# Optimization experiments

Measured on AMD Instinct MI355X. Metric: run time of the kernel, lower is better.

The kernel has to match this reference:

```python
import jax, jax.numpy as jnp
import numpy as np

N_NODES = 50000


def gcn_conv(x, W, b, src, dst, n):
    # dense transform first (as PyG GCNConv does), then sparse aggregate
    h = x @ W  # [N, out]
    # add self loops
    loop = jnp.arange(n, dtype=src.dtype)
    s = jnp.concatenate([src, loop])
    d = jnp.concatenate([dst, loop])
    # symmetric normalization: deg over targets with unit edge weights
    deg = jax.ops.segment_sum(jnp.ones_like(d, dtype=h.dtype), d, num_segments=n)
    dinv = jnp.where(deg > 0, jax.lax.rsqrt(deg), 0.0)
    norm = dinv[s] * dinv[d]  # [E+N]
    msg = h[s] * norm[:, None]  # gather + scale
    out = jax.ops.segment_sum(msg, d, num_segments=n)  # scatter-add
    return out + b


def setup_inputs() -> dict:
    key = jax.random.key(0)
    k1, k2, k3, k4, k5 = jax.random.split(key, 5)
    in_dim, hid, out_dim = 256, 128, 16
    x = jax.random.normal(k1, (N_NODES, in_dim), dtype=jnp.float32)
    edge_index = jax.random.randint(k2, (2, 800000), 0, N_NODES, dtype=jnp.int64)
    # Glorot-style init for GCNConv weights, zero bias (PyG default)
    W1 = jax.random.normal(k3, (in_dim, hid), dtype=jnp.float32) / np.sqrt(in_dim)
    b1 = jnp.zeros((hid,), dtype=jnp.float32)
    W2 = jax.random.normal(k4, (hid, out_dim), dtype=jnp.float32) / np.sqrt(hid)
    b2 = jnp.zeros((out_dim,), dtype=jnp.float32)
    return {"x": x, "edge_index": edge_index, "W1": W1, "b1": b1, "W2": W2, "b2": b2}


def reference(x, edge_index, W1, b1, W2, b2):
    # eval-mode forward: dropout is identity
    src, dst = edge_index[0], edge_index[1]
    n = x.shape[0]
    h = gcn_conv(x, W1, b1, src, dst, n)
    h = jax.nn.relu(h)
    h = gcn_conv(h, W2, b2, src, dst, n)
    return jax.nn.log_softmax(h, axis=1)
```

## Files before the change

### kernel.cpp

```cpp
#include <hip/hip_runtime.h>
#include <hip/hip_bf16.h>

#define N_NODES 50000
#define E_EDGES 800000
#define IN_DIM  256
#define HID     128
#define OUT_DIM 16

#define NBUCK 391
#define NBLK  128
#define P2CAP 4096

using frag_ab = __attribute__((ext_vector_type(8))) short;
using frag_cd = __attribute__((ext_vector_type(4))) float;

static __device__ inline short f2bf(float f) {
    union { float f; unsigned u; } v; v.f = f;
    unsigned r = (v.u + 0x7fffu + ((v.u >> 16) & 1u)) >> 16;
    return (short)r;
}
static __device__ inline float bflo(unsigned u) {
    union { unsigned u; float f; } v; v.u = u << 16; return v.f;
}
static __device__ inline float bfhi(unsigned u) {
    union { unsigned u; float f; } v; v.u = u & 0xffff0000u; return v.f;
}
static __device__ inline unsigned packbf(float a, float b) {
    return (unsigned)(unsigned short)f2bf(a) | ((unsigned)(unsigned short)f2bf(b) << 16);
}


__global__ __launch_bounds__(256) void csr_a(const int4* __restrict__ dst4,
                                             int* __restrict__ cnt_bb) {
    __shared__ int h[NBUCK];
    int t = threadIdx.x;
    for (int i = t; i < NBUCK; i += 256) h[i] = 0;
    __syncthreads();
    for (int i = blockIdx.x * 256 + t; i < E_EDGES / 4; i += NBLK * 256) {
        int4 d = dst4[i];
        atomicAdd(&h[d.x >> 7], 1);
        atomicAdd(&h[d.y >> 7], 1);
        atomicAdd(&h[d.z >> 7], 1);
        atomicAdd(&h[d.w >> 7], 1);
    }
    __syncthreads();
    for (int i = t; i < NBUCK; i += 256) cnt_bb[i * NBLK + blockIdx.x] = h[i];
}

__global__ __launch_bounds__(NBLK) void csr_b1(int* __restrict__ cnt_bb,
                                               int* __restrict__ btot) {
    __shared__ int sm[NBLK];
    int b = blockIdx.x, t = threadIdx.x;
    int v = cnt_bb[b * NBLK + t];
    sm[t] = v;
    __syncthreads();
    for (int o = 1; o < NBLK; o <<= 1) {
        int u = (t >= o) ? sm[t - o] : 0;
        __syncthreads();
        sm[t] += u;
        __syncthreads();
    }
    cnt_bb[b * NBLK + t] = sm[t] - v;
    if (t == NBLK - 1) btot[b] = sm[t];
}

__global__ __launch_bounds__(512) void csr_b2_w1t(const int* __restrict__ btot,
                                                  int* __restrict__ bbase,
                                                  const float* __restrict__ W,
                                                  uint4* __restrict__ wtf,
                                                  const float* __restrict__ W2,
                                                  short* __restrict__ w2t) {
    int t = threadIdx.x;
    if (blockIdx.x < 8) {
        int j = blockIdx.x * 512 + t;
        int f = j >> 6, lane = j & 63;
        int kt = f >> 3, tt = f & 7;
        int m = lane & 15, q = lane >> 4;
        int c = tt * 16 + m;
        int k0 = kt * 32 + q * 8;
        unsigned p[4];
#pragma unroll
        for (int i = 0; i < 4; ++i)
            p[i] = packbf(W[(k0 + 2 * i) * HID + c], W[(k0 + 2 * i + 1) * HID + c]);
        uint4 v; v.x = p[0]; v.y = p[1]; v.z = p[2]; v.w = p[3];
        wtf[j] = v;
        return;
    }
    if (blockIdx.x == 9) {
        int n0 = t >> 5, k0 = (t & 31) * 4;
#pragma unroll
        for (int i = 0; i < 4; ++i)
            w2t[n0 * HID + k0 + i] = f2bf(W2[(k0 + i) * OUT_DIM + n0]);
        return;
    }
    __shared__ int sm[512];
    int v = (t < NBUCK) ? btot[t] : 0;
    sm[t] = v;
    __syncthreads();
    for (int o = 1; o < 512; o <<= 1) {
        int u = (t >= o) ? sm[t - o] : 0;
        __syncthreads();
        sm[t] += u;
        __syncthreads();
    }
    if (t < NBUCK) bbase[t] = sm[t] - v;
    if (t == 511) bbase[NBUCK] = sm[511];
}

__global__ __launch_bounds__(256) void csr_c(const int4* __restrict__ src4,
                                             const int4* __restrict__ dst4,
                                             const int* __restrict__ cnt_bb,
                                             const int* __restrict__ bbase,
                                             unsigned* __restrict__ tmp) {
    __shared__ int run[NBUCK];
    int t = threadIdx.x;
    for (int i = t; i < NBUCK; i += 256)
        run[i] = bbase[i] + cnt_bb[i * NBLK + blockIdx.x];
    __syncthreads();
    for (int i = blockIdx.x * 256 + t; i < E_EDGES / 4; i += NBLK * 256) {
        int4 d = dst4[i];
        int4 s = src4[i];
        int p0 = atomicAdd(&run[d.x >> 7], 1);
        tmp[p0] = (unsigned)s.x | ((unsigned)(d.x & 127) << 17);
        int p1 = atomicAdd(&run[d.y >> 7], 1);
        tmp[p1] = (unsigned)s.y | ((unsigned)(d.y & 127) << 17);
        int p2 = atomicAdd(&run[d.z >> 7], 1);
        tmp[p2] = (unsigned)s.z | ((unsigned)(d.z & 127) << 17);
        int p3 = atomicAdd(&run[d.w >> 7], 1);
        tmp[p3] = (unsigned)s.w | ((unsigned)(d.w & 127) << 17);
    }
}

__global__ __launch_bounds__(256) void csr_p2(const unsigned* __restrict__ tmp,
                                              const int* __restrict__ bbase,
                                              int* __restrict__ rowptr,
                                              float* __restrict__ dinv,
                                              int* __restrict__ ssrc) {
    __shared__ unsigned ed[P2CAP];
    __shared__ int cnt[128];
    __shared__ int off[128];
    int b = blockIdx.x, t = threadIdx.x;
    int base = bbase[b];
    int m = bbase[b + 1] - base;
    if (m > P2CAP) m = P2CAP;
    if (t < 128) cnt[t] = 0;
    __syncthreads();
    for (int i = t; i < m; i += 256) {
        unsigned v = tmp[base + i];
        ed[i] = v;
        atomicAdd(&cnt[v >> 17], 1);
    }
    __syncthreads();
    if (t < 128) off[t] = cnt[t];
    __syncthreads();
    for (int o = 1; o < 128; o <<= 1) {
        int u = (t >= o && t < 128) ? off[t - o] : 0;
        __syncthreads();
        if (t < 128) off[t] += u;
        __syncthreads();
    }
    if (t < 128) {
        int node = b * 128 + t;
        int ex = off[t] - cnt[t];
        if (node < N_NODES) {
            rowptr[node] = base + ex;
            dinv[node] = rsqrtf((float)(cnt[t] + 1));
        }
        off[t] = ex;
    }
    if (b == NBUCK - 1 && t == 0) rowptr[N_NODES] = E_EDGES;
    __syncthreads();
    for (int i = t; i < m; i += 256) {
        unsigned v = ed[i];
        int p = atomicAdd(&off[v >> 17], 1);
        ssrc[base + p] = (int)(v & 0x1FFFF);
    }
}

__global__ __launch_bounds__(512) void gemm1_mfma(const float* __restrict__ x,
                                                  const uint4* __restrict__ wtf,
                                                  const float* __restrict__ dinv,
                                                  short* __restrict__ h) {
    __shared__ uint4 lwt[64 * 64];
    int tid = threadIdx.x;
#pragma unroll
    for (int i = 0; i < 8; ++i)
        lwt[i * 512 + tid] = wtf[i * 512 + tid];

    int wave = tid >> 6;
    int lane = tid & 63;
    int m = lane & 15;
    int q = lane >> 4;
    int row0 = blockIdx.x * 128 + wave * 16;
    int arow_idx = row0 + m;
    const float4* arow4 = (const float4*)(x + (size_t)(arow_idx < N_NODES ? arow_idx : 0) * IN_DIM);

    frag_ab a[8];
#pragma unroll
    for (int kt = 0; kt < 8; ++kt) {
        float4 f0 = arow4[kt * 8 + q * 2];
        float4 f1 = arow4[kt * 8 + q * 2 + 1];
        a[kt][0] = f2bf(f0.x); a[kt][1] = f2bf(f0.y); a[kt][2] = f2bf(f0.z); a[kt][3] = f2bf(f0.w);
        a[kt][4] = f2bf(f1.x); a[kt][5] = f2bf(f1.y); a[kt][6] = f2bf(f1.z); a[kt][7] = f2bf(f1.w);
    }

    frag_cd acc[8];
#pragma unroll
    for (int t = 0; t < 8; ++t) acc[t] = frag_cd{0.f, 0.f, 0.f, 0.f};

    __syncthreads();

#pragma unroll
    for (int kt = 0; kt < 8; ++kt) {
#pragma unroll
        for (int t = 0; t < 8; ++t) {
            frag_ab b = *(const frag_ab*)&lwt[(kt * 8 + t) * 64 + lane];
            acc[t] = __builtin_amdgcn_mfma_f32_16x16x32_bf16(a[kt], b, acc[t], 0, 0, 0);
        }
    }

    float dv[4];
#pragma unroll
    for (int r = 0; r < 4; ++r) {
        int orow = row0 + q * 4 + r;
        dv[r] = (orow < N_NODES) ? dinv[orow] : 0.f;
    }
#pragma unroll
    for (int t = 0; t < 8; ++t) {
#pragma unroll
        for (int r = 0; r < 4; ++r) {
            int orow = row0 + q * 4 + r;
            if (orow < N_NODES)
                h[(size_t)orow * HID + t * 16 + m] = f2bf(acc[t][r] * dv[r]);
        }
    }
}

__global__ __launch_bounds__(256) void agg1_pull(const short* __restrict__ h1s,
                                                 const float* __restrict__ dinv,
                                                 const float* __restrict__ b1,
                                                 const int* __restrict__ rowptr,
                                                 const int* __restrict__ ssrc,
                                                 uint4* __restrict__ out1) {
    int wave = threadIdx.x >> 6;
    int lane = threadIdx.x & 63;
    int slot  = blockIdx.x & 7;
    int nb    = blockIdx.x >> 3;
    int slice = slot >> 1;
    int half  = slot & 1;
    int node = __builtin_amdgcn_readfirstlane(nb * 8 + half * 4 + wave);
    if (node >= N_NODES) return;
    int eo = lane >> 2;
    int g  = lane & 3;

    const short* base = h1s + slice * 32 + g * 8;
    int lo = rowptr[node], hi = rowptr[node + 1];
    float dd = dinv[node];
    float a0 = 0.f, a1 = 0.f, a2 = 0.f, a3 = 0.f;
    float a4 = 0.f, a5 = 0.f, a6 = 0.f, a7 = 0.f;

    if (eo == 0) {
        uint4 u = *(const uint4*)(base + (size_t)node * HID);
        a0 = bflo(u.x); a1 = bfhi(u.x); a2 = bflo(u.y); a3 = bfhi(u.y);
        a4 = bflo(u.z); a5 = bfhi(u.z); a6 = bflo(u.w); a7 = bfhi(u.w);
    }

    int e = lo;
    for (; e + 32 <= hi; e += 32) {
        int s0 = ssrc[e + eo];
        int s1 = ssrc[e + 16 + eo];
        uint4 u0 = *(const uint4*)(base + (size_t)s0 * HID);
        uint4 u1 = *(const uint4*)(base + (size_t)s1 * HID);
        a0 += bflo(u0.x); a1 += bfhi(u0.x); a2 += bflo(u0.y); a3 += bfhi(u0.y);
        a4 += bflo(u0.z); a5 += bfhi(u0.z); a6 += bflo(u0.w); a7 += bfhi(u0.w);
        a0 += bflo(u1.x); a1 += bfhi(u1.x); a2 += bflo(u1.y); a3 += bfhi(u1.y);
        a4 += bflo(u1.z); a5 += bfhi(u1.z); a6 += bflo(u1.w); a7 += bfhi(u1.w);
    }
    for (; e + 16 <= hi; e += 16) {
        int s = ssrc[e + eo];
        uint4 u = *(const uint4*)(base + (size_t)s * HID);
        a0 += bflo(u.x); a1 += bfhi(u.x); a2 += bflo(u.y); a3 += bfhi(u.y);
        a4 += bflo(u.z); a5 += bfhi(u.z); a6 += bflo(u.w); a7 += bfhi(u.w);
    }
    if (eo < hi - e) {
        int s = ssrc[e + eo];
        uint4 u = *(const uint4*)(base + (size_t)s * HID);
        a0 += bflo(u.x); a1 += bfhi(u.x); a2 += bflo(u.y); a3 += bfhi(u.y);
        a4 += bflo(u.z); a5 += bfhi(u.z); a6 += bflo(u.w); a7 += bfhi(u.w);
    }

#pragma unroll
    for (int msk = 4; msk <= 32; msk <<= 1) {
        a0 += __shfl_xor(a0, msk); a1 += __shfl_xor(a1, msk);
        a2 += __shfl_xor(a2, msk); a3 += __shfl_xor(a3, msk);
        a4 += __shfl_xor(a4, msk); a5 += __shfl_xor(a5, msk);
        a6 += __shfl_xor(a6, msk); a7 += __shfl_xor(a7, msk);
    }

    if (eo == 0) {
        const float* bs = b1 + slice * 32 + g * 8;
        float4 bA = *(const float4*)bs;
        float4 bB = *(const float4*)(bs + 4);
        float o0 = fmaxf(fmaf(dd, a0, bA.x), 0.f);
        float o1 = fmaxf(fmaf(dd, a1, bA.y), 0.f);
        float o2 = fmaxf(fmaf(dd, a2, bA.z), 0.f);
        float o3 = fmaxf(fmaf(dd, a3, bA.w), 0.f);
        float o4 = fmaxf(fmaf(dd, a4, bB.x), 0.f);
        float o5 = fmaxf(fmaf(dd, a5, bB.y), 0.f);
        float o6 = fmaxf(fmaf(dd, a6, bB.z), 0.f);
        float o7 = fmaxf(fmaf(dd, a7, bB.w), 0.f);
        uint4 st;
        st.x = packbf(o0, o1); st.y = packbf(o2, o3);
        st.z = packbf(o4, o5); st.w = packbf(o6, o7);
        out1[(size_t)node * 16 + slice * 4 + g] = st;
    }
}

__global__ __launch_bounds__(256) void gemm2_mfma(const short* __restrict__ out1,
                                                  const short* __restrict__ w2t,
                                                  const float* __restrict__ dinv,
                                                  short* __restrict__ h2s) {
    int wave = threadIdx.x >> 6;
    int lane = threadIdx.x & 63;
    int m = lane & 15;
    int q = lane >> 4;
    int row0 = blockIdx.x * 64 + wave * 16;
    int arow = row0 + m;
    if (arow >= N_NODES) arow = N_NODES - 1;
    const short* ap = out1 + (size_t)arow * HID + q * 8;
    const short* bp = w2t + m * HID + q * 8;

    frag_cd acc = frag_cd{0.f, 0.f, 0.f, 0.f};
#pragma unroll
    for (int kt = 0; kt < 4; ++kt) {
        frag_ab a = *(const frag_ab*)(ap + kt * 32);
        frag_ab b = *(const frag_ab*)(bp + kt * 32);
        acc = __builtin_amdgcn_mfma_f32_16x16x32_bf16(a, b, acc, 0, 0, 0);
    }
#pragma unroll
    for (int r = 0; r < 4; ++r) {
        int row = row0 + q * 4 + r;
        if (row < N_NODES)
            h2s[(size_t)row * OUT_DIM + m] = f2bf(acc[r] * dinv[row]);
    }
}

__global__ __launch_bounds__(256) void agg2_pull(const unsigned* __restrict__ h2s,
                                                 const float* __restrict__ dinv,
                                                 const float* __restrict__ b2,
                                                 const int* __restrict__ rowptr,
                                                 const int* __restrict__ ssrc,
                                                 float* __restrict__ out) {
    int wave = threadIdx.x >> 6;
    int lane = threadIdx.x & 63;
    int node = __builtin_amdgcn_readfirstlane(blockIdx.x * 4 + wave);
    if (node >= N_NODES) return;
    int eo = lane >> 3;
    int g  = lane & 7;

    int lo = rowptr[node], hi = rowptr[node + 1];
    float a0 = 0.f, a1 = 0.f;
    if (eo == 0) {
        unsigned u = h2s[(size_t)node * 8 + g];
        a0 = bflo(u); a1 = bfhi(u);
    }
    int e = lo;
    for (; e + 16 <= hi; e += 16) {
        int s0 = ssrc[e + eo];
        int s1 = ssrc[e + 8 + eo];
        unsigned u0 = h2s[(size_t)s0 * 8 + g];
        unsigned u1 = h2s[(size_t)s1 * 8 + g];
        a0 += bflo(u0); a1 += bfhi(u0);
        a0 += bflo(u1); a1 += bfhi(u1);
    }
    for (; e + 8 <= hi; e += 8) {
        int s = ssrc[e + eo];
        unsigned u = h2s[(size_t)s * 8 + g];
        a0 += bflo(u); a1 += bfhi(u);
    }
    if (eo < hi - e) {
        int s = ssrc[e + eo];
        unsigned u = h2s[(size_t)s * 8 + g];
        a0 += bflo(u); a1 += bfhi(u);
    }

    a0 += __shfl_xor(a0, 8);  a1 += __shfl_xor(a1, 8);
    a0 += __shfl_xor(a0, 16); a1 += __shfl_xor(a1, 16);
    a0 += __shfl_xor(a0, 32); a1 += __shfl_xor(a1, 32);

    float dd = dinv[node];
    float2 bb = *(const float2*)(b2 + 2 * g);
    float v0 = fmaf(dd, a0, bb.x);
    float v1 = fmaf(dd, a1, bb.y);

    float m = fmaxf(v0, v1);
#pragma unroll
    for (int msk = 1; msk < 8; msk <<= 1) m = fmaxf(m, __shfl_xor(m, msk));
    float s2 = __expf(v0 - m) + __expf(v1 - m);
#pragma unroll
    for (int msk = 1; msk < 8; msk <<= 1) s2 += __shfl_xor(s2, msk);
    float lse = m + __logf(s2);
    if (eo == 0) {
        float2 o; o.x = v0 - lse; o.y = v1 - lse;
        *(float2*)(out + (size_t)node * OUT_DIM + 2 * g) = o;
    }
}

extern "C" void kernel_launch(void* const* d_in, const int* in_sizes, int n_in,
                              void* d_out, int out_size, void* d_ws, size_t ws_size,
                              hipStream_t stream) {
    const float* x  = (const float*)d_in[0];
    const int*   ei = (const int*)d_in[1];
    const float* W1 = (const float*)d_in[2];
    const float* b1 = (const float*)d_in[3];
    const float* W2 = (const float*)d_in[4];
    const float* b2 = (const float*)d_in[5];
    float* out = (float*)d_out;

    const int n = N_NODES;
    const int e = E_EDGES;
    const int* srcp = ei;
    const int* dstp = ei + e;

    char* w = (char*)d_ws;
    int*      cnt_bb = (int*)w;        w += (size_t)NBUCK * NBLK * 4;
    int*      btot   = (int*)w;        w += (size_t)NBUCK * 4;
    int*      bbase  = (int*)w;        w += (size_t)(NBUCK + 1) * 4;
    int*      rowptr = (int*)w;        w += (size_t)(n + 1) * 4;
    float*    dinv   = (float*)w;      w += (size_t)n * 4;
    unsigned* tmp    = (unsigned*)w;   w += (size_t)e * 4;
    int*      ssrc   = (int*)w;        w += (size_t)e * 4;
    uint4*    wtf    = (uint4*)w;      w += (size_t)64 * 64 * 16;
    short*    w2t    = (short*)w;      w += (size_t)OUT_DIM * HID * 2;
    short*    h1s    = (short*)w;      w += (size_t)n * HID * 2;
    short*    out1   = (short*)w;      w += (size_t)n * HID * 2;
    short*    h2s    = (short*)w;      w += (size_t)n * OUT_DIM * 2;

    auto blk = [](long long total, int b) { return (int)((total + b - 1) / b); };

    csr_a<<<NBLK, 256, 0, stream>>>((const int4*)dstp, cnt_bb);
    csr_b1<<<NBUCK, NBLK, 0, stream>>>(cnt_bb, btot);
    csr_b2_w1t<<<10, 512, 0, stream>>>(btot, bbase, W1, wtf, W2, w2t);
    csr_c<<<NBLK, 256, 0, stream>>>((const int4*)srcp, (const int4*)dstp, cnt_bb, bbase, tmp);
    csr_p2<<<NBUCK, 256, 0, stream>>>(tmp, bbase, rowptr, dinv, ssrc);

    gemm1_mfma<<<blk(n, 128), 512, 0, stream>>>(x, wtf, dinv, h1s);
    agg1_pull<<<6250 * 8, 256, 0, stream>>>(h1s, dinv, b1, rowptr, ssrc, (uint4*)out1);

    gemm2_mfma<<<blk(n, 64), 256, 0, stream>>>(out1, w2t, dinv, h2s);
    agg2_pull<<<blk(n, 4), 256, 0, stream>>>((const unsigned*)h2s, dinv, b2, rowptr, ssrc, out);
}
```

Before: 226.8 us.

## Rework aggregation kernels: full-row gathers for node pairs, wider agg2 loads

agg1_pull now has each wave handle two nodes, with 16 lanes covering a full 128-wide bf16 row. Previously eight blocks each covered a 32-column slice of a node. This cuts redundant rowptr/ssrc reads and the launch count, and gives each edge a full 256-byte contiguous gather, but only 4 edges per node are in flight per iteration. agg2_pull switches to 8-byte loads with 16 edges per iteration and does the 16-wide softmax across 4 lanes.

```diff
diff --git a/kernel.cpp b/kernel.cpp
--- a/kernel.cpp
+++ b/kernel.cpp
@@ -244,75 +244,97 @@
                                                  uint4* __restrict__ out1) {
     int wave = threadIdx.x >> 6;
     int lane = threadIdx.x & 63;
-    int slot  = blockIdx.x & 7;
-    int nb    = blockIdx.x >> 3;
-    int slice = slot >> 1;
-    int half  = slot & 1;
-    int node = __builtin_amdgcn_readfirstlane(nb * 8 + half * 4 + wave);
-    if (node >= N_NODES) return;
-    int eo = lane >> 2;
-    int g  = lane & 3;
-
-    const short* base = h1s + slice * 32 + g * 8;
-    int lo = rowptr[node], hi = rowptr[node + 1];
-    float dd = dinv[node];
+    int pair = __builtin_amdgcn_readfirstlane(blockIdx.x * 4 + wave);
+    int n0 = pair * 2;
+    if (n0 >= N_NODES) return;
+    int n1 = n0 + 1;
+    int eo = lane >> 4;
+    int g  = lane & 15;
+
+    int lo0 = rowptr[n0];
+    int mid = rowptr[n0 + 1];
+    int hi1 = rowptr[n1 + 1];
+    float dd0 = dinv[n0], dd1 = dinv[n1];
+
     float a0 = 0.f, a1 = 0.f, a2 = 0.f, a3 = 0.f;
     float a4 = 0.f, a5 = 0.f, a6 = 0.f, a7 = 0.f;
+    float c0 = 0.f, c1 = 0.f, c2 = 0.f, c3 = 0.f;
+    float c4 = 0.f, c5 = 0.f, c6 = 0.f, c7 = 0.f;
 
     if (eo == 0) {
-        uint4 u = *(const uint4*)(base + (size_t)node * HID);
+        uint4 u = *(const uint4*)(h1s + (size_t)n0 * HID + g * 8);
         a0 = bflo(u.x); a1 = bfhi(u.x); a2 = bflo(u.y); a3 = bfhi(u.y);
         a4 = bflo(u.z); a5 = bfhi(u.z); a6 = bflo(u.w); a7 = bfhi(u.w);
-    }
-
-    int e = lo;
-    for (; e + 32 <= hi; e += 32) {
-        int s0 = ssrc[e + eo];
-        int s1 = ssrc[e + 16 + eo];
-        uint4 u0 = *(const uint4*)(base + (size_t)s0 * HID);
-        uint4 u1 = *(const uint4*)(base + (size_t)s1 * HID);
+    } else if (eo == 1) {
+        uint4 u = *(const uint4*)(h1s + (size_t)n1 * HID + g * 8);
+        c0 = bflo(u.x); c1 = bfhi(u.x); c2 = bflo(u.y); c3 = bfhi(u.y);
+        c4 = bflo(u.z); c5 = bfhi(u.z); c6 = bflo(u.w); c7 = bfhi(u.w);
+    }
+
+    int e0 = lo0, e1 = mid;
+    for (; e0 + 4 <= mid && e1 + 4 <= hi1; e0 += 4, e1 += 4) {
+        int s0 = ssrc[e0 + eo];
+        int s1 = ssrc[e1 + eo];
+        uint4 u0 = *(const uint4*)(h1s + (size_t)s0 * HID + g * 8);
+        uint4 u1 = *(const uint4*)(h1s + (size_t)s1 * HID + g * 8);
         a0 += bflo(u0.x); a1 += bfhi(u0.x); a2 += bflo(u0.y); a3 += bfhi(u0.y);
         a4 += bflo(u0.z); a5 += bfhi(u0.z); a6 += bflo(u0.w); a7 += bfhi(u0.w);
-        a0 += bflo(u1.x); a1 += bfhi(u1.x); a2 += bflo(u1.y); a3 += bfhi(u1.y);
-        a4 += bflo(u1.z); a5 += bfhi(u1.z); a6 += bflo(u1.w); a7 += bfhi(u1.w);
-    }
-    for (; e + 16 <= hi; e += 16) {
-        int s = ssrc[e + eo];
-        uint4 u = *(const uint4*)(base + (size_t)s * HID);
+        c0 += bflo(u1.x); c1 += bfhi(u1.x); c2 += bflo(u1.y); c3 += bfhi(u1.y);
+        c4 += bflo(u1.z); c5 += bfhi(u1.z); c6 += bflo(u1.w); c7 += bfhi(u1.w);
+    }
+    for (; e0 + 4 <= mid; e0 += 4) {
+        int s = ssrc[e0 + eo];
+        uint4 u = *(const uint4*)(h1s + (size_t)s * HID + g * 8);
         a0 += bflo(u.x); a1 += bfhi(u.x); a2 += bflo(u.y); a3 += bfhi(u.y);
         a4 += bflo(u.z); a5 += bfhi(u.z); a6 += bflo(u.w); a7 += bfhi(u.w);
     }
-    if (eo < hi - e) {
-        int s = ssrc[e + eo];
-        uint4 u = *(const uint4*)(base + (size_t)s * HID);
+    for (; e1 + 4 <= hi1; e1 += 4) {
+        int s = ssrc[e1 + eo];
+        uint4 u = *(const uint4*)(h1s + (size_t)s * HID + g * 8);
+        c0 += bflo(u.x); c1 += bfhi(u.x); c2 += bflo(u.y); c3 += bfhi(u.y);
+        c4 += bflo(u.z); c5 += bfhi(u.z); c6 += bflo(u.w); c7 += bfhi(u.w);
+    }
+    if (eo < mid - e0) {
+        int s = ssrc[e0 + eo];
+        uint4 u = *(const uint4*)(h1s + (size_t)s * HID + g * 8);
         a0 += bflo(u.x); a1 += bfhi(u.x); a2 += bflo(u.y); a3 += bfhi(u.y);
         a4 += bflo(u.z); a5 += bfhi(u.z); a6 += bflo(u.w); a7 += bfhi(u.w);
     }
-
-#pragma unroll
-    for (int msk = 4; msk <= 32; msk <<= 1) {
+    if (eo < hi1 - e1) {
+        int s = ssrc[e1 + eo];
+        uint4 u = *(const uint4*)(h1s + (size_t)s * HID + g * 8);
+        c0 += bflo(u.x); c1 += bfhi(u.x); c2 += bflo(u.y); c3 += bfhi(u.y);
+        c4 += bflo(u.z); c5 += bfhi(u.z); c6 += bflo(u.w); c7 += bfhi(u.w);
+    }
+
+#pragma unroll
+    for (int msk = 16; msk <= 32; msk <<= 1) {
         a0 += __shfl_xor(a0, msk); a1 += __shfl_xor(a1, msk);
         a2 += __shfl_xor(a2, msk); a3 += __shfl_xor(a3, msk);
         a4 += __shfl_xor(a4, msk); a5 += __shfl_xor(a5, msk);
         a6 += __shfl_xor(a6, msk); a7 += __shfl_xor(a7, msk);
-    }
-
+        c0 += __shfl_xor(c0, msk); c1 += __shfl_xor(c1, msk);
+        c2 += __shfl_xor(c2, msk); c3 += __shfl_xor(c3, msk);
+        c4 += __shfl_xor(c4, msk); c5 += __shfl_xor(c5, msk);
+        c6 += __shfl_xor(c6, msk); c7 += __shfl_xor(c7, msk);
+    }
+
+    float4 bA = *(const float4*)(b1 + g * 8);
+    float4 bB = *(const float4*)(b1 + g * 8 + 4);
     if (eo == 0) {
-        const float* bs = b1 + slice * 32 + g * 8;
-        float4 bA = *(const float4*)bs;
-        float4 bB = *(const float4*)(bs + 4);
-        float o0 = fmaxf(fmaf(dd, a0, bA.x), 0.f);
-        float o1 = fmaxf(fmaf(dd, a1, bA.y), 0.f);
-        float o2 = fmaxf(fmaf(dd, a2, bA.z), 0.f);
-        float o3 = fmaxf(fmaf(dd, a3, bA.w), 0.f);
-        float o4 = fmaxf(fmaf(dd, a4, bB.x), 0.f);
-        float o5 = fmaxf(fmaf(dd, a5, bB.y), 0.f);
-        float o6 = fmaxf(fmaf(dd, a6, bB.z), 0.f);
-        float o7 = fmaxf(fmaf(dd, a7, bB.w), 0.f);
         uint4 st;
-        st.x = packbf(o0, o1); st.y = packbf(o2, o3);
-        st.z = packbf(o4, o5); st.w = packbf(o6, o7);
-        out1[(size_t)node * 16 + slice * 4 + g] = st;
+        st.x = packbf(fmaxf(fmaf(dd0, a0, bA.x), 0.f), fmaxf(fmaf(dd0, a1, bA.y), 0.f));
+        st.y = packbf(fmaxf(fmaf(dd0, a2, bA.z), 0.f), fmaxf(fmaf(dd0, a3, bA.w), 0.f));
+        st.z = packbf(fmaxf(fmaf(dd0, a4, bB.x), 0.f), fmaxf(fmaf(dd0, a5, bB.y), 0.f));
+        st.w = packbf(fmaxf(fmaf(dd0, a6, bB.z), 0.f), fmaxf(fmaf(dd0, a7, bB.w), 0.f));
+        out1[(size_t)n0 * 16 + g] = st;
+    } else if (eo == 1) {
+        uint4 st;
+        st.x = packbf(fmaxf(fmaf(dd1, c0, bA.x), 0.f), fmaxf(fmaf(dd1, c1, bA.y), 0.f));
+        st.y = packbf(fmaxf(fmaf(dd1, c2, bA.z), 0.f), fmaxf(fmaf(dd1, c3, bA.w), 0.f));
+        st.z = packbf(fmaxf(fmaf(dd1, c4, bB.x), 0.f), fmaxf(fmaf(dd1, c5, bB.y), 0.f));
+        st.w = packbf(fmaxf(fmaf(dd1, c6, bB.z), 0.f), fmaxf(fmaf(dd1, c7, bB.w), 0.f));
+        out1[(size_t)n1 * 16 + g] = st;
     }
 }
 
@@ -345,7 +367,7 @@
     }
 }
 
-__global__ __launch_bounds__(256) void agg2_pull(const unsigned* __restrict__ h2s,
+__global__ __launch_bounds__(256) void agg2_pull(const uint2* __restrict__ h2s2,
                                                  const float* __restrict__ dinv,
                                                  const float* __restrict__ b2,
                                                  const int* __restrict__ rowptr,
@@ -355,54 +377,50 @@
     int lane = threadIdx.x & 63;
     int node = __builtin_amdgcn_readfirstlane(blockIdx.x * 4 + wave);
     if (node >= N_NODES) return;
-    int eo = lane >> 3;
-    int g  = lane & 7;
+    int eo = lane >> 2;
+    int g  = lane & 3;
 
     int lo = rowptr[node], hi = rowptr[node + 1];
-    float a0 = 0.f, a1 = 0.f;
+    float a0 = 0.f, a1 = 0.f, a2 = 0.f, a3 = 0.f;
     if (eo == 0) {
-        unsigned u = h2s[(size_t)node * 8 + g];
-        a0 = bflo(u); a1 = bfhi(u);
+        uint2 u = h2s2[(size_t)node * 4 + g];
+        a0 = bflo(u.x); a1 = bfhi(u.x); a2 = bflo(u.y); a3 = bfhi(u.y);
     }
     int e = lo;
     for (; e + 16 <= hi; e += 16) {
-        int s0 = ssrc[e + eo];
-        int s1 = ssrc[e + 8 + eo];
-        unsigned u0 = h2s[(size_t)s0 * 8 + g];
-        unsigned u1 = h2s[(size_t)s1 * 8 + g];
-        a0 += bflo(u0); a1 += bfhi(u0);
-        a0 += bflo(u1); a1 += bfhi(u1);
-    }
-    for (; e + 8 <= hi; e += 8) {
         int s = ssrc[e + eo];
-        unsigned u = h2s[(size_t)s * 8 + g];
-        a0 += bflo(u); a1 += bfhi(u);
+        uint2 u = h2s2[(size_t)s * 4 + g];
+        a0 += bflo(u.x); a1 += bfhi(u.x); a2 += bflo(u.y); a3 += bfhi(u.y);
     }
     if (eo < hi - e) {
         int s = ssrc[e + eo];
-        unsigned u = h2s[(size_t)s * 8 + g];
-        a0 += bflo(u); a1 += bfhi(u);
-    }
-
-    a0 += __shfl_xor(a0, 8);  a1 += __shfl_xor(a1, 8);
-    a0 += __shfl_xor(a0, 16); a1 += __shfl_xor(a1, 16);
-    a0 += __shfl_xor(a0, 32); a1 += __shfl_xor(a1, 32);
+        uint2 u = h2s2[(size_t)s * 4 + g];
+        a0 += bflo(u.x); a1 += bfhi(u.x); a2 += bflo(u.y); a3 += bfhi(u.y);
+    }
+
+#pragma unroll
+    for (int msk = 4; msk <= 32; msk <<= 1) {
+        a0 += __shfl_xor(a0, msk); a1 += __shfl_xor(a1, msk);
+        a2 += __shfl_xor(a2, msk); a3 += __shfl_xor(a3, msk);
+    }
 
     float dd = dinv[node];
-    float2 bb = *(const float2*)(b2 + 2 * g);
+    float4 bb = *(const float4*)(b2 + 4 * g);
     float v0 = fmaf(dd, a0, bb.x);
     float v1 = fmaf(dd, a1, bb.y);
-
-    float m = fmaxf(v0, v1);
-#pragma unroll
-    for (int msk = 1; msk < 8; msk <<= 1) m = fmaxf(m, __shfl_xor(m, msk));
-    float s2 = __expf(v0 - m) + __expf(v1 - m);
-#pragma unroll
-    for (int msk = 1; msk < 8; msk <<= 1) s2 += __shfl_xor(s2, msk);
-    float lse = m + __logf(s2);
+    float v2 = fmaf(dd, a2, bb.z);
+    float v3 = fmaf(dd, a3, bb.w);
+
+    float m = fmaxf(fmaxf(v0, v1), fmaxf(v2, v3));
+    m = fmaxf(m, __shfl_xor(m, 1));
+    m = fmaxf(m, __shfl_xor(m, 2));
+    float s4 = __expf(v0 - m) + __expf(v1 - m) + __expf(v2 - m) + __expf(v3 - m);
+    s4 += __shfl_xor(s4, 1);
+    s4 += __shfl_xor(s4, 2);
+    float lse = m + __logf(s4);
     if (eo == 0) {
-        float2 o; o.x = v0 - lse; o.y = v1 - lse;
-        *(float2*)(out + (size_t)node * OUT_DIM + 2 * g) = o;
+        float4 o; o.x = v0 - lse; o.y = v1 - lse; o.z = v2 - lse; o.w = v3 - lse;
+        *(float4*)(out + (size_t)node * OUT_DIM + 4 * g) = o;
     }
 }
 
@@ -445,8 +463,8 @@
     csr_p2<<<NBUCK, 256, 0, stream>>>(tmp, bbase, rowptr, dinv, ssrc);
 
     gemm1_mfma<<<blk(n, 128), 512, 0, stream>>>(x, wtf, dinv, h1s);
-    agg1_pull<<<6250 * 8, 256, 0, stream>>>(h1s, dinv, b1, rowptr, ssrc, (uint4*)out1);
+    agg1_pull<<<blk(n / 2, 4), 256, 0, stream>>>(h1s, dinv, b1, rowptr, ssrc, (uint4*)out1);
 
     gemm2_mfma<<<blk(n, 64), 256, 0, stream>>>(out1, w2t, dinv, h2s);
-    agg2_pull<<<blk(n, 4), 256, 0, stream>>>((const unsigned*)h2s, dinv, b2, rowptr, ssrc, out);
-}
+    agg2_pull<<<blk(n, 4), 256, 0, stream>>>((const uint2*)h2s, dinv, b2, rowptr, ssrc, out);
+}
```

Measured after the change: 190.8 us. 1.19x faster.
